# Kernel tuning notes

Hardware: AMD Instinct MI355X
Metric: run time of the kernel (lower is better)

The kernel has to match this reference:

```python
import jax, jax.numpy as jnp
import numpy as np

B, N, H, E, WF = 2048, 30, 256, 256, 32
TANH_C = 10.0  # tanh_exploration


def _mask_modify(m):
    # if a row is all True, un-mask the last column
    all_true = jnp.all(m, axis=1)
    return m.at[:, -1].set(m[:, -1] & ~all_true)


def _lstm_cell(x, h, c, W_ih, W_hh, b_ih, b_hh):
    gates = x @ W_ih.T + b_ih + h @ W_hh.T + b_hh
    i, f, g, o = jnp.split(gates, 4, axis=1)  # torch LSTMCell gate order
    c_new = jax.nn.sigmoid(f) * c + jax.nn.sigmoid(i) * jnp.tanh(g)
    h_new = jax.nn.sigmoid(o) * jnp.tanh(c_new)
    return h_new, c_new


def _attention(query, ref, Wq, bq, Wr, br, v, C=None):
    # query [B,H], ref [B,H,N] (context permuted)
    q = query @ Wq.T + bq                                        # [B,H]
    e = jnp.einsum('oh,bhn->bon', Wr, ref) + br[None, :, None]   # 1x1 conv
    u = jnp.einsum('h,bhn->bn', v, jnp.tanh(q[:, :, None] + e))  # [B,N]
    logits = C * jnp.tanh(u) if C is not None else u
    return e, logits


def setup_inputs() -> dict:
    key = jax.random.key(0)
    ks = jax.random.split(key, 24)
    s = 0.06  # ~1/sqrt(H) init scale
    n = lambda k, sh: jax.random.normal(k, sh, dtype=jnp.float32)
    return {
        'decoder_input': n(ks[0], (B, E)),
        'embedded_inputs': n(ks[1], (N, B, E)),
        'h0': n(ks[2], (B, H)),
        'c0': n(ks[3], (B, H)),
        'context': n(ks[4], (N, B, H)),
        'embed_cou': n(ks[5], (B, WF)),
        'D': jax.random.uniform(ks[6], (B, N, N), dtype=jnp.float32),
        'W_ih': n(ks[7], (4 * H, E)) * s,
        'W_hh': n(ks[8], (4 * H, H)) * s,
        'b_ih': n(ks[9], (4 * H,)) * s,
        'b_hh': n(ks[10], (4 * H,)) * s,
        'W_merge': n(ks[11], (H, H + WF)) * s,
        'b_merge': n(ks[12], (H,)) * s,
        'Wq_p': n(ks[13], (H, H)) * s,
        'bq_p': n(ks[14], (H,)) * s,
        'Wr_p': n(ks[15], (H, H)) * s,
        'br_p': n(ks[16], (H,)) * s,
        'v_p': n(ks[17], (H,)) * s,
        'Wq_g': n(ks[18], (H, H)) * s,
        'bq_g': n(ks[19], (H,)) * s,
        'Wr_g': n(ks[20], (H, H)) * s,
        'br_g': n(ks[21], (H,)) * s,
        'v_g': n(ks[22], (H,)) * s,
        'V_reach_mask_t': jnp.zeros((B, N), dtype=bool),
        'start_idx': jax.random.randint(ks[23], (B,), 0, N),
        'k_min_nodes': 3,
    }


def reference(decoder_input, embedded_inputs, h0, c0, context, embed_cou, D,
              W_ih, W_hh, b_ih, b_hh, W_merge, b_merge,
              Wq_p, bq_p, Wr_p, br_p, v_p,
              Wq_g, bq_g, Wr_g, br_g, v_g,
              V_reach_mask_t, start_idx, k_min_nodes):
    ref = jnp.transpose(context, (1, 2, 0))  # [B,H,N]
    arangeB = jnp.arange(B)
    arangeN = jnp.arange(N)

    def step(carry, _):
        h, c, mask, idxs, dec_in, knn_row = carry
        # --- update_knn_mask ('n-1'): builds the row used at the NEXT step ---
        Eb = D[arangeB, idxs]                                  # [B,N]
        weighted = Eb * (~mask).astype(Eb.dtype)
        valid = jnp.sum(~mask, axis=1) > k_min_nodes
        far = jnp.argmax(weighted, axis=1)
        next_row = (arangeN[None, :] == far[:, None]) & valid[:, None]
        # --- recurrence: update_mask + check_mask ---
        lm = mask.at[arangeB, idxs].set(True)
        lm = _mask_modify(_mask_modify(lm))
        full_mask = lm | knn_row
        # LSTM step + worker-feature merge
        hy, cy = _lstm_cell(dec_in, h, c, W_ih, W_hh, b_ih, b_hh)
        g_l = jnp.concatenate([hy, embed_cou], axis=1) @ W_merge.T + b_merge
        # one glimpse (n_glimpses=1)
        e_g, lg = _attention(g_l, ref, Wq_g, bq_g, Wr_g, br_g, v_g)
        lg = jnp.where(full_mask, -jnp.inf, lg)
        g_l = jnp.einsum('bhn,bn->bh', e_g, jax.nn.softmax(lg, axis=1))
        # pointer (use_tanh with C)
        _, lp = _attention(g_l, ref, Wq_p, bq_p, Wr_p, br_p, v_p, C=TANH_C)
        lp = jnp.where(full_mask, -jnp.inf, lp)
        log_p = jax.nn.log_softmax(lp, axis=1)
        new_idxs = jnp.argmax(log_p, axis=1)  # greedy decode
        new_dec = embedded_inputs[new_idxs, arangeB]  # [B,E]
        return (hy, cy, lm, new_idxs, new_dec, next_row), (log_p, new_idxs)

    init = (h0, c0, V_reach_mask_t, start_idx, decoder_input,
            jnp.zeros_like(V_reach_mask_t))
    (_, _, mask, _, _, _), (logps, sels) = jax.lax.scan(step, init, None, length=N)
    return jnp.swapaxes(logps, 0, 1), jnp.swapaxes(sels, 0, 1), mask
```

## Files before the change

### kernel.cpp

```cpp
#include <hip/hip_runtime.h>
#include <hip/hip_bf16.h>
#include <math.h>

#define B 2048
#define NN 30
#define H 256
#define EDIM 256
#define G4 1024

typedef __attribute__((ext_vector_type(8))) short short8;
typedef __attribute__((ext_vector_type(4))) float f32x4;

__device__ __forceinline__ float fsig(float x) {
    return __fdividef(1.f, 1.f + __expf(-x));
}
__device__ __forceinline__ float ftanh(float x) {
    return 1.f - __fdividef(2.f, __expf(2.f * x) + 1.f);
}

__device__ __forceinline__ void split3(float a, unsigned short& h,
                                       unsigned short& m_, unsigned short& l_)
{
    unsigned ab = __float_as_uint(a);
    h = (unsigned short)(ab >> 16);
    float r1 = a - __uint_as_float(ab & 0xffff0000u);
    unsigned rb = __float_as_uint(r1);
    m_ = (unsigned short)(rb >> 16);
    float r2 = r1 - __uint_as_float(rb & 0xffff0000u);
    l_ = (unsigned short)(__float_as_uint(r2) >> 16);
}

__global__ __launch_bounds__(256)
void gemm_big(const float* __restrict__ A,
              const float* __restrict__ W0, const float* __restrict__ W1,
              const float* __restrict__ W2,
              const float* __restrict__ b0, const float* __restrict__ b1,
              const float* __restrict__ b2,
              float* __restrict__ C0, float* __restrict__ C1,
              float* __restrict__ C2)
{
    __shared__ __align__(16) unsigned short Ah[128][40];
    __shared__ __align__(16) unsigned short Am[128][40];
    __shared__ __align__(16) unsigned short Al[128][40];
    __shared__ __align__(16) unsigned short Bh[128][40];
    __shared__ __align__(16) unsigned short Bm[128][40];
    __shared__ __align__(16) unsigned short Bl[128][40];

    int tid = threadIdx.x;
    int w = tid >> 6, l = tid & 63;

    int lin = blockIdx.y * 6 + blockIdx.x;
    int v = (lin & 7) * 360 + (lin >> 3);
    int m0 = (v / 6) << 7;
    int nblk = v % 6;
    int part = nblk >> 1;
    int nin = (nblk & 1) << 7;
    const float* W    = part == 0 ? W0 : part == 1 ? W1 : W2;
    const float* bias = part == 0 ? b0 : part == 1 ? b1 : b2;
    float* C          = part == 0 ? C0 : part == 1 ? C1 : C2;

    int srow = tid >> 1;
    int skb  = (tid & 1) << 4;
    const float* arow = A + (long)(m0 + srow) * 256 + skb;
    const float* wrow = W + (long)(nin + srow) * 256 + skb;

    int fr = l & 15;
    int fk = (l >> 4) << 3;

    f32x4 acc[2][8];
    #pragma unroll
    for (int i = 0; i < 2; ++i)
        #pragma unroll
        for (int j = 0; j < 8; ++j)
            acc[i][j] = (f32x4){0.f, 0.f, 0.f, 0.f};

    for (int kt = 0; kt < 8; ++kt) {
        int k0 = kt << 5;
        float4 a4[4], w4[4];
        #pragma unroll
        for (int i = 0; i < 4; ++i) {
            a4[i] = *(const float4*)(arow + k0 + (i << 2));
            w4[i] = *(const float4*)(wrow + k0 + (i << 2));
        }
        __syncthreads();
        #pragma unroll
        for (int i = 0; i < 4; ++i) {
            float va[4] = {a4[i].x, a4[i].y, a4[i].z, a4[i].w};
            float vw[4] = {w4[i].x, w4[i].y, w4[i].z, w4[i].w};
            #pragma unroll
            for (int j = 0; j < 4; ++j) {
                int c = skb + (i << 2) + j;
                split3(va[j], Ah[srow][c], Am[srow][c], Al[srow][c]);
                split3(vw[j], Bh[srow][c], Bm[srow][c], Bl[srow][c]);
            }
        }
        __syncthreads();

        short8 aH[2], aM[2], aL[2];
        #pragma unroll
        for (int ms = 0; ms < 2; ++ms) {
            int r = (w << 5) + (ms << 4) + fr;
            aH[ms] = *(const short8*)&Ah[r][fk];
            aM[ms] = *(const short8*)&Am[r][fk];
            aL[ms] = *(const short8*)&Al[r][fk];
        }
        #pragma unroll
        for (int ng = 0; ng < 2; ++ng) {
            short8 bH[4], bM[4], bL[4];
            #pragma unroll
            for (int j = 0; j < 4; ++j) {
                int r = (((ng << 2) + j) << 4) + fr;
                bH[j] = *(const short8*)&Bh[r][fk];
                bM[j] = *(const short8*)&Bm[r][fk];
                bL[j] = *(const short8*)&Bl[r][fk];
            }
            #pragma unroll
            for (int ms = 0; ms < 2; ++ms)
                #pragma unroll
                for (int j = 0; j < 4; ++j)
                    acc[ms][(ng << 2) + j] = __builtin_amdgcn_mfma_f32_16x16x32_bf16(
                        aH[ms], bH[j], acc[ms][(ng << 2) + j], 0, 0, 0);
            #pragma unroll
            for (int ms = 0; ms < 2; ++ms)
                #pragma unroll
                for (int j = 0; j < 4; ++j)
                    acc[ms][(ng << 2) + j] = __builtin_amdgcn_mfma_f32_16x16x32_bf16(
                        aH[ms], bM[j], acc[ms][(ng << 2) + j], 0, 0, 0);
            #pragma unroll
            for (int ms = 0; ms < 2; ++ms)
                #pragma unroll
                for (int j = 0; j < 4; ++j)
                    acc[ms][(ng << 2) + j] = __builtin_amdgcn_mfma_f32_16x16x32_bf16(
                        aM[ms], bH[j], acc[ms][(ng << 2) + j], 0, 0, 0);
            #pragma unroll
            for (int ms = 0; ms < 2; ++ms)
                #pragma unroll
                for (int j = 0; j < 4; ++j)
                    acc[ms][(ng << 2) + j] = __builtin_amdgcn_mfma_f32_16x16x32_bf16(
                        aH[ms], bL[j], acc[ms][(ng << 2) + j], 0, 0, 0);
            #pragma unroll
            for (int ms = 0; ms < 2; ++ms)
                #pragma unroll
                for (int j = 0; j < 4; ++j)
                    acc[ms][(ng << 2) + j] = __builtin_amdgcn_mfma_f32_16x16x32_bf16(
                        aM[ms], bM[j], acc[ms][(ng << 2) + j], 0, 0, 0);
            #pragma unroll
            for (int ms = 0; ms < 2; ++ms)
                #pragma unroll
                for (int j = 0; j < 4; ++j)
                    acc[ms][(ng << 2) + j] = __builtin_amdgcn_mfma_f32_16x16x32_bf16(
                        aL[ms], bH[j], acc[ms][(ng << 2) + j], 0, 0, 0);
        }
    }

    #pragma unroll
    for (int ms = 0; ms < 2; ++ms) {
        #pragma unroll
        for (int ns = 0; ns < 8; ++ns) {
            float bv = bias[nin + (ns << 4) + fr];
            #pragma unroll
            for (int r = 0; r < 4; ++r) {
                int m = m0 + (w << 5) + (ms << 4) + ((l >> 4) << 2) + r;
                C[(long)m * 256 + nin + (ns << 4) + fr] = acc[ms][ns][r] + bv;
            }
        }
    }
}

__global__ __launch_bounds__(256)
void gates_mfma(const unsigned short* __restrict__ dhi, const unsigned short* __restrict__ dlo,
                const unsigned short* __restrict__ hhi, const unsigned short* __restrict__ hlo,
                const unsigned short* __restrict__ Whi, const unsigned short* __restrict__ Wlo,
                const float* __restrict__ bsum, const float* __restrict__ cin,
                float* __restrict__ hout, float* __restrict__ cout,
                unsigned short* __restrict__ hohi, unsigned short* __restrict__ holo)
{
    __shared__ __align__(16) unsigned short Ah[128][40];
    __shared__ __align__(16) unsigned short Al[128][40];
    __shared__ __align__(16) unsigned short Bh[64][40];
    __shared__ __align__(16) unsigned short Bl[64][40];

    int tid = threadIdx.x;
    int w = tid >> 6, l = tid & 63;
    int lin = blockIdx.x;
    int v = (lin & 7) * 32 + (lin >> 3);
    int m0 = (v >> 4) << 7;
    int u0 = (v & 15) << 4;

    int arow = tid >> 1;
    int akb  = (tid & 1) << 4;
    int brw  = tid >> 2;
    int bkb  = (tid & 3) << 3;
    int wrow = ((brw >> 4) << 8) + u0 + (brw & 15);
    const unsigned short* wph = Whi + (long)wrow * 512 + bkb;
    const unsigned short* wpl = Wlo + (long)wrow * 512 + bkb;

    int fk = (l >> 4) << 3;
    int fr = l & 15;

    f32x4 acc[2][4];
    #pragma unroll
    for (int i = 0; i < 2; ++i)
        #pragma unroll
        for (int j = 0; j < 4; ++j)
            acc[i][j] = (f32x4){0.f, 0.f, 0.f, 0.f};

    for (int kt = 0; kt < 16; ++kt) {
        int k0 = kt << 5;
        const unsigned short* sah; const unsigned short* sal; int kk;
        if (k0 < 256) { sah = dhi; sal = dlo; kk = k0; }
        else          { sah = hhi; sal = hlo; kk = k0 - 256; }
        long abase = (long)(m0 + arow) * 256 + kk + akb;
        short8 a0 = *(const short8*)&sah[abase];
        short8 a1 = *(const short8*)&sah[abase + 8];
        short8 a2 = *(const short8*)&sal[abase];
        short8 a3 = *(const short8*)&sal[abase + 8];
        short8 b0 = *(const short8*)&wph[k0];
        short8 b1 = *(const short8*)&wpl[k0];
        __syncthreads();
        *(short8*)&Ah[arow][akb]     = a0;
        *(short8*)&Ah[arow][akb + 8] = a1;
        *(short8*)&Al[arow][akb]     = a2;
        *(short8*)&Al[arow][akb + 8] = a3;
        *(short8*)&Bh[brw][bkb] = b0;
        *(short8*)&Bl[brw][bkb] = b1;
        __syncthreads();

        short8 aH[2], aL[2], bH[4], bL[4];
        #pragma unroll
        for (int ms = 0; ms < 2; ++ms) {
            int r = (w << 5) + (ms << 4) + fr;
            aH[ms] = *(const short8*)&Ah[r][fk];
            aL[ms] = *(const short8*)&Al[r][fk];
        }
        #pragma unroll
        for (int s = 0; s < 4; ++s) {
            int r = (s << 4) + fr;
            bH[s] = *(const short8*)&Bh[r][fk];
            bL[s] = *(const short8*)&Bl[r][fk];
        }
        #pragma unroll
        for (int ms = 0; ms < 2; ++ms)
            #pragma unroll
            for (int s = 0; s < 4; ++s)
                acc[ms][s] = __builtin_amdgcn_mfma_f32_16x16x32_bf16(aH[ms], bH[s], acc[ms][s], 0, 0, 0);
        #pragma unroll
        for (int ms = 0; ms < 2; ++ms)
            #pragma unroll
            for (int s = 0; s < 4; ++s)
                acc[ms][s] = __builtin_amdgcn_mfma_f32_16x16x32_bf16(aH[ms], bL[s], acc[ms][s], 0, 0, 0);
        #pragma unroll
        for (int ms = 0; ms < 2; ++ms)
            #pragma unroll
            for (int s = 0; s < 4; ++s)
                acc[ms][s] = __builtin_amdgcn_mfma_f32_16x16x32_bf16(aL[ms], bH[s], acc[ms][s], 0, 0, 0);
    }

    int u = u0 + fr;
    float bI = bsum[u], bF = bsum[256 + u], bG = bsum[512 + u], bO = bsum[768 + u];
    #pragma unroll
    for (int ms = 0; ms < 2; ++ms) {
        #pragma unroll
        for (int r = 0; r < 4; ++r) {
            int m = m0 + (w << 5) + (ms << 4) + ((l >> 4) << 2) + r;
            float gi = acc[ms][0][r] + bI;
            float gf = acc[ms][1][r] + bF;
            float gg = acc[ms][2][r] + bG;
            float go = acc[ms][3][r] + bO;
            float cv = cin[(long)m * H + u];
            float cn = fsig(gf) * cv + fsig(gi) * ftanh(gg);
            float hn = fsig(go) * ftanh(cn);
            cout[(long)m * H + u] = cn;
            hout[(long)m * H + u] = hn;
            unsigned hb = __float_as_uint(hn);
            hohi[(long)m * H + u] = (unsigned short)(hb >> 16);
            float lo = hn - __uint_as_float(hb & 0xffff0000u);
            holo[(long)m * H + u] = (unsigned short)(__float_as_uint(lo) >> 16);
        }
    }
}

__global__ __launch_bounds__(256)
void gemm_qg(const float* __restrict__ A, const float* __restrict__ W,
             const float* __restrict__ addend, float* __restrict__ C)
{
    __shared__ __align__(16) float As[2][16][36];
    __shared__ __align__(16) float Ws[2][16][68];
    int tid = threadIdx.x;
    int tx = tid & 15, ty = tid >> 4;

    int lin = blockIdx.y * 4 + blockIdx.x;
    int v = (lin & 7) * 32 + (lin >> 3);
    int m0 = (v >> 2) << 5;
    int n0 = (v & 3) << 6;

    int lrA = tid >> 3, lkA = (tid & 7) << 1;
    int lrW = tid >> 2, lkW = (tid & 3) << 2;
    const float* arow = A + (long)(m0 + lrA) * 256;
    const float* wrow = W + (long)(n0 + lrW) * 256;

    float2 av = *(const float2*)(arow + lkA);
    float4 wv = *(const float4*)(wrow + lkW);
    As[0][lkA + 0][lrA] = av.x; As[0][lkA + 1][lrA] = av.y;
    Ws[0][lkW + 0][lrW] = wv.x; Ws[0][lkW + 1][lrW] = wv.y;
    Ws[0][lkW + 2][lrW] = wv.z; Ws[0][lkW + 3][lrW] = wv.w;
    __syncthreads();

    float acc[2][4] = {};
    int p = 0;
    for (int k0 = 0; k0 < 256; k0 += 16) {
        float2 nav; float4 nwv;
        bool more = (k0 + 16) < 256;
        if (more) {
            nav = *(const float2*)(arow + k0 + 16 + lkA);
            nwv = *(const float4*)(wrow + k0 + 16 + lkW);
        }
        #pragma unroll
        for (int k = 0; k < 16; ++k) {
            float2 a2 = *(const float2*)&As[p][k][ty << 1];
            float4 b4 = *(const float4*)&Ws[p][k][tx << 2];
            acc[0][0] = fmaf(a2.x, b4.x, acc[0][0]);
            acc[0][1] = fmaf(a2.x, b4.y, acc[0][1]);
            acc[0][2] = fmaf(a2.x, b4.z, acc[0][2]);
            acc[0][3] = fmaf(a2.x, b4.w, acc[0][3]);
            acc[1][0] = fmaf(a2.y, b4.x, acc[1][0]);
            acc[1][1] = fmaf(a2.y, b4.y, acc[1][1]);
            acc[1][2] = fmaf(a2.y, b4.z, acc[1][2]);
            acc[1][3] = fmaf(a2.y, b4.w, acc[1][3]);
        }
        if (more) {
            int q = p ^ 1;
            As[q][lkA + 0][lrA] = nav.x; As[q][lkA + 1][lrA] = nav.y;
            Ws[q][lkW + 0][lrW] = nwv.x; Ws[q][lkW + 1][lrW] = nwv.y;
            Ws[q][lkW + 2][lrW] = nwv.z; Ws[q][lkW + 3][lrW] = nwv.w;
        }
        __syncthreads();
        p ^= 1;
    }

    #pragma unroll
    for (int i = 0; i < 2; ++i) {
        int m = m0 + (ty << 1) + i;
        const float* ad = &addend[(long)m * 256 + n0 + (tx << 2)];
        float4 adv = *(const float4*)ad;
        float4 o = make_float4(acc[i][0] + adv.x, acc[i][1] + adv.y,
                               acc[i][2] + adv.z, acc[i][3] + adv.w);
        *(float4*)&C[(long)m * 256 + n0 + (tx << 2)] = o;
    }
}

__global__ void init_state(const unsigned char* __restrict__ vr, const int* __restrict__ start,
                           unsigned char* __restrict__ mask, unsigned char* __restrict__ knn,
                           int* __restrict__ idxs)
{
    int t = blockIdx.x * 256 + threadIdx.x;
    if (t < B * NN) { mask[t] = vr[t] ? 1 : 0; knn[t] = 0; }
    if (t < B) idxs[t] = start[t];
}

__global__ void prep_wsplit(const float* __restrict__ Wih, const float* __restrict__ Whh,
                            const float* __restrict__ bih, const float* __restrict__ bhh,
                            unsigned short* __restrict__ Whi, unsigned short* __restrict__ Wlo,
                            float* __restrict__ bsum)
{
    int n = blockIdx.x, k = threadIdx.x;
    float a = Wih[(long)n * H + k];
    unsigned ab = __float_as_uint(a);
    Whi[(long)n * 512 + k] = (unsigned short)(ab >> 16);
    float alo = a - __uint_as_float(ab & 0xffff0000u);
    Wlo[(long)n * 512 + k] = (unsigned short)(__float_as_uint(alo) >> 16);
    float b = Whh[(long)n * H + k];
    unsigned bb = __float_as_uint(b);
    Whi[(long)n * 512 + 256 + k] = (unsigned short)(bb >> 16);
    float blo = b - __uint_as_float(bb & 0xffff0000u);
    Wlo[(long)n * 512 + 256 + k] = (unsigned short)(__float_as_uint(blo) >> 16);
    if (k == 0) bsum[n] = bih[n] + bhh[n];
}

__global__ void conv_pair(const float* __restrict__ x,
                          unsigned short* __restrict__ xhi, unsigned short* __restrict__ xlo)
{
    int t = blockIdx.x * 256 + threadIdx.x;
    float a = x[t];
    unsigned ab = __float_as_uint(a);
    xhi[t] = (unsigned short)(ab >> 16);
    float lo = a - __uint_as_float(ab & 0xffff0000u);
    xlo[t] = (unsigned short)(__float_as_uint(lo) >> 16);
}

__global__ void prep_compose1(const float* __restrict__ Wqg, const float* __restrict__ Wm,
                              float* __restrict__ W1c)
{
    int h = blockIdx.x, k = threadIdx.x;
    float a = 0.f;
    for (int j = 0; j < H; ++j) a = fmaf(Wqg[(long)h * H + j], Wm[(long)j * 288 + k], a);
    W1c[(long)h * H + k] = a;
}

__global__ void prep_compose2(const float* __restrict__ Wqg, const float* __restrict__ Wm,
                              const float* __restrict__ bm, const float* __restrict__ bqg,
                              float* __restrict__ W2c, float* __restrict__ bc)
{
    int h = blockIdx.x, w = threadIdx.x;
    if (w < 32) {
        float a = 0.f;
        for (int j = 0; j < H; ++j) a = fmaf(Wqg[(long)h * H + j], Wm[(long)j * 288 + 256 + w], a);
        W2c[h * 32 + w] = a;
    } else if (w == 32) {
        float a = 0.f;
        for (int j = 0; j < H; ++j) a = fmaf(Wqg[(long)h * H + j], bm[j], a);
        bc[h] = a + bqg[h];
    }
}

__global__ __launch_bounds__(256)
void prep_qc(const float* __restrict__ cou, const float* __restrict__ W2c,
             const float* __restrict__ bc, float* __restrict__ qc)
{
    __shared__ float sWT[32 * 256];
    __shared__ float sb[256];
    int b = blockIdx.x, h = threadIdx.x;
    for (int i = h; i < 32 * 256; i += 256) {
        int hh = i >> 5, ww = i & 31;
        sWT[ww * 256 + hh] = W2c[i];
    }
    sb[h] = bc[h];
    __syncthreads();
    const float* cr = cou + (long)b * 32;
    float a = sb[h];
    for (int w = 0; w < 32; ++w) a = fmaf(cr[w], sWT[w * 256 + h], a);
    qc[(long)b * H + h] = a;
}

__global__ void prep_composeF(const float* __restrict__ Wqp, const float* __restrict__ Wrg,
                              const float* __restrict__ brg, float* __restrict__ WFc,
                              float* __restrict__ bFc)
{
    int f = blockIdx.x, k = threadIdx.x;
    float a = 0.f;
    for (int j = 0; j < H; ++j) a = fmaf(Wqp[(long)f * H + j], Wrg[(long)j * H + k], a);
    WFc[(long)f * H + k] = a;
    if (k == 0) {
        float s = 0.f;
        for (int j = 0; j < H; ++j) s = fmaf(Wqp[(long)f * H + j], brg[j], s);
        bFc[f] = s;
    }
}

__global__ __launch_bounds__(512)
void mega_attn2(const float* __restrict__ eg, const float* __restrict__ ep,
                const float* __restrict__ F, const float* __restrict__ qg,
                const float* __restrict__ vg, const float* __restrict__ vp,
                const float* __restrict__ bqp,
                const float* __restrict__ D, const int* __restrict__ kminp,
                unsigned char* __restrict__ mask, unsigned char* __restrict__ knn,
                const float* __restrict__ emb,
                float* __restrict__ out, int step,
                int* __restrict__ idxs,
                unsigned short* __restrict__ dechi, unsigned short* __restrict__ declo)
{
    int b = blockIdx.x, tid = threadIdx.x;
    int wv = tid >> 6, lane = tid & 63;
    __shared__ float sU[32], sP[32];
    __shared__ float sQp[H];
    __shared__ float sPar[2][H];
    __shared__ unsigned char sFull[32];
    __shared__ int sSel;

    float4 q4  = ((const float4*)(qg + (long)b * H))[lane];
    float4 vg4 = ((const float4*)vg)[lane];
    float4 vp4 = ((const float4*)vp)[lane];

    if (tid < 64) {
        bool in = lane < NN;
        int idx = idxs[b];
        int kmin = *kminp;
        unsigned char m = in ? mask[b * NN + lane] : (unsigned char)1;
        float dv = in ? D[((long)b * NN + idx) * NN + lane] : 0.f;
        unsigned long long unm = __ballot(in && !m);
        int cnt = __popcll(unm);
        bool valid = cnt > kmin;
        float bw = (in && !m) ? dv : (in ? 0.f : -1.f);
        int bi = in ? lane : 1000;
        #pragma unroll
        for (int off = 32; off; off >>= 1) {
            float ow = __shfl_down(bw, off, 64);
            int oi = __shfl_down(bi, off, 64);
            if (ow > bw || (ow == bw && oi < bi)) { bw = ow; bi = oi; }
        }
        int far = __shfl(bi, 0, 64);
        unsigned char mnew = (in && lane == idx) ? 1 : m;
        #pragma unroll
        for (int rep = 0; rep < 2; ++rep) {
            bool allm = (__ballot(in && !mnew) == 0ull);
            if (allm && lane == NN - 1) mnew = 0;
        }
        unsigned char kn = in ? knn[b * NN + lane] : 0;
        if (in) {
            sFull[lane] = (mnew | kn) ? 1 : 0;
            mask[b * NN + lane] = mnew;
            knn[b * NN + lane] = (lane == far && valid) ? 1 : 0;
        }
    }
    __syncthreads();

    for (int n = wv; n < NN; n += 8) {
        if (sFull[n]) continue;
        float4 e4 = ((const float4*)(eg + ((long)n * B + b) * H))[lane];
        float s = vg4.x * ftanh(q4.x + e4.x);
        s = fmaf(vg4.y, ftanh(q4.y + e4.y), s);
        s = fmaf(vg4.z, ftanh(q4.z + e4.z), s);
        s = fmaf(vg4.w, ftanh(q4.w + e4.w), s);
        #pragma unroll
        for (int off = 32; off; off >>= 1) s += __shfl_down(s, off, 64);
        if (lane == 0) sU[n] = s;
    }
    __syncthreads();

    if (tid < 64) {
        bool in = tid < NN;
        bool f = in ? (sFull[tid] != 0) : true;
        float u = (in && !f) ? sU[tid] : -INFINITY;
        float mx = u;
        #pragma unroll
        for (int off = 32; off; off >>= 1) mx = fmaxf(mx, __shfl_down(mx, off, 64));
        mx = __shfl(mx, 0, 64);
        float p = (in && !f) ? __expf(u - mx) : 0.f;
        float sum = p;
        #pragma unroll
        for (int off = 32; off; off >>= 1) sum += __shfl_down(sum, off, 64);
        sum = __shfl(sum, 0, 64);
        if (in) sP[tid] = p / sum;
    }
    __syncthreads();

    {
        int half = tid >> 8, hh = tid & 255;
        float a = 0.f;
        #pragma unroll
        for (int n = 0; n < 15; ++n) {
            int nn = half * 15 + n;
            float pn = sP[nn];
            if (pn != 0.f)
                a = fmaf(pn, F[((long)nn * B + b) * H + hh], a);
        }
        sPar[half][hh] = a;
    }
    __syncthreads();
    if (tid < 256) sQp[tid] = bqp[tid] + sPar[0][tid] + sPar[1][tid];
    __syncthreads();

    float4 qp4 = ((const float4*)sQp)[lane];
    for (int n = wv; n < NN; n += 8) {
        if (sFull[n]) continue;
        float4 e4 = ((const float4*)(ep + ((long)n * B + b) * H))[lane];
        float s = vp4.x * ftanh(qp4.x + e4.x);
        s = fmaf(vp4.y, ftanh(qp4.y + e4.y), s);
        s = fmaf(vp4.z, ftanh(qp4.z + e4.z), s);
        s = fmaf(vp4.w, ftanh(qp4.w + e4.w), s);
        #pragma unroll
        for (int off = 32; off; off >>= 1) s += __shfl_down(s, off, 64);
        if (lane == 0) sU[n] = 10.f * ftanh(s);
    }
    __syncthreads();

    if (tid < 64) {
        bool in = tid < NN;
        bool f = in ? (sFull[tid] != 0) : true;
        float l = (in && !f) ? sU[tid] : -INFINITY;
        float mx = l; int bi = in ? tid : 1000;
        #pragma unroll
        for (int off = 32; off; off >>= 1) {
            float om = __shfl_down(mx, off, 64);
            int oi = __shfl_down(bi, off, 64);
            if (om > mx || (om == mx && oi < bi)) { mx = om; bi = oi; }
        }
        mx = __shfl(mx, 0, 64);
        bi = __shfl(bi, 0, 64);
        float pe = (in && !f) ? __expf(l - mx) : 0.f;
        float sum = pe;
        #pragma unroll
        for (int off = 32; off; off >>= 1) sum += __shfl_down(sum, off, 64);
        sum = __shfl(sum, 0, 64);
        float lse = mx + __logf(sum);
        if (tid == 0) {
            idxs[b] = bi;
            out[(long)B * NN * NN + (long)b * NN + step] = (float)bi;
            sSel = bi;
        }
        if (in)
            out[(long)b * NN * NN + (long)step * NN + tid] =
                f ? -1e30f : (l - lse);
    }
    __syncthreads();

    if (tid < 256) {
        int sel = sSel;
        float d = emb[((long)sel * B + b) * EDIM + tid];
        unsigned db = __float_as_uint(d);
        dechi[(long)b * H + tid] = (unsigned short)(db >> 16);
        float lo = d - __uint_as_float(db & 0xffff0000u);
        declo[(long)b * H + tid] = (unsigned short)(__float_as_uint(lo) >> 16);
    }
}

__global__ void mask_out(const unsigned char* __restrict__ mask, float* __restrict__ out)
{
    int t = blockIdx.x * 256 + threadIdx.x;
    if (t < B * NN)
        out[(long)B * NN * NN + (long)B * NN + t] = mask[t] ? 1.f : 0.f;
}

extern "C" void kernel_launch(void* const* d_in, const int* in_sizes, int n_in,
                              void* d_out, int out_size, void* d_ws, size_t ws_size,
                              hipStream_t stream)
{
    const float* decoder_input = (const float*)d_in[0];
    const float* embedded     = (const float*)d_in[1];
    const float* h0           = (const float*)d_in[2];
    const float* c0           = (const float*)d_in[3];
    const float* context      = (const float*)d_in[4];
    const float* embed_cou    = (const float*)d_in[5];
    const float* D            = (const float*)d_in[6];
    const float* W_ih         = (const float*)d_in[7];
    const float* W_hh         = (const float*)d_in[8];
    const float* b_ih         = (const float*)d_in[9];
    const float* b_hh         = (const float*)d_in[10];
    const float* W_merge      = (const float*)d_in[11];
    const float* b_merge      = (const float*)d_in[12];
    const float* Wq_p         = (const float*)d_in[13];
    const float* bq_p         = (const float*)d_in[14];
    const float* Wr_p         = (const float*)d_in[15];
    const float* br_p         = (const float*)d_in[16];
    const float* v_p          = (const float*)d_in[17];
    const float* Wq_g         = (const float*)d_in[18];
    const float* bq_g         = (const float*)d_in[19];
    const float* Wr_g         = (const float*)d_in[20];
    const float* br_g         = (const float*)d_in[21];
    const float* v_g          = (const float*)d_in[22];
    const unsigned char* vreach = (const unsigned char*)d_in[23];
    const int* start_idx      = (const int*)d_in[24];
    const int* kminp          = (const int*)d_in[25];

    float* ws = (float*)d_ws;
    size_t o = 0;
    float* eg     = ws + o; o += (size_t)B * NN * H;
    float* ep     = ws + o; o += (size_t)B * NN * H;
    float* Fbuf   = ws + o; o += (size_t)B * NN * H;
    float* hb0    = ws + o; o += (size_t)B * H;
    float* hb1    = ws + o; o += (size_t)B * H;
    float* cb0    = ws + o; o += (size_t)B * H;
    float* cb1    = ws + o; o += (size_t)B * H;
    float* qbuf   = ws + o; o += (size_t)B * H;
    float* qc     = ws + o; o += (size_t)B * H;
    float* W1c    = ws + o; o += (size_t)H * H;
    float* W2c    = ws + o; o += (size_t)H * 32;
    float* bc     = ws + o; o += (size_t)H;
    float* WFc    = ws + o; o += (size_t)H * H;
    float* bFc    = ws + o; o += (size_t)H;
    float* bsum   = ws + o; o += (size_t)G4;
    unsigned short* Whi  = (unsigned short*)(ws + o); o += (size_t)G4 * 512 / 2;
    unsigned short* Wlo  = (unsigned short*)(ws + o); o += (size_t)G4 * 512 / 2;
    unsigned short* dechi = (unsigned short*)(ws + o); o += (size_t)B * H / 2;
    unsigned short* declo = (unsigned short*)(ws + o); o += (size_t)B * H / 2;
    unsigned short* hAhi = (unsigned short*)(ws + o); o += (size_t)B * H / 2;
    unsigned short* hAlo = (unsigned short*)(ws + o); o += (size_t)B * H / 2;
    unsigned short* hBhi = (unsigned short*)(ws + o); o += (size_t)B * H / 2;
    unsigned short* hBlo = (unsigned short*)(ws + o); o += (size_t)B * H / 2;
    unsigned char* maskb = (unsigned char*)(ws + o);
    unsigned char* knnb  = maskb + (size_t)B * NN;
    int* idxs = (int*)(knnb + (size_t)B * NN + 64);

    float* out = (float*)d_out;

    init_state<<<dim3((B * NN + 255) / 256), dim3(256), 0, stream>>>(
        vreach, start_idx, maskb, knnb, idxs);

    prep_wsplit<<<dim3(G4), dim3(256), 0, stream>>>(W_ih, W_hh, b_ih, b_hh,
                                                    Whi, Wlo, bsum);
    conv_pair<<<dim3(B * H / 256), dim3(256), 0, stream>>>(decoder_input, dechi, declo);
    conv_pair<<<dim3(B * H / 256), dim3(256), 0, stream>>>(h0, hAhi, hAlo);
    prep_compose1<<<dim3(H), dim3(256), 0, stream>>>(Wq_g, W_merge, W1c);
    prep_compose2<<<dim3(H), dim3(64), 0, stream>>>(Wq_g, W_merge, b_merge, bq_g,
                                                    W2c, bc);
    prep_qc<<<dim3(B), dim3(256), 0, stream>>>(embed_cou, W2c, bc, qc);
    prep_composeF<<<dim3(H), dim3(256), 0, stream>>>(Wq_p, Wr_g, br_g, WFc, bFc);

    gemm_big<<<dim3(6, (B * NN) / 128), dim3(256), 0, stream>>>(
        context, Wr_g, Wr_p, WFc, br_g, br_p, bFc, eg, ep, Fbuf);

    const float* cin = c0;
    unsigned short* hInHi = hAhi; unsigned short* hInLo = hAlo;
    unsigned short* hOutHi = hBhi; unsigned short* hOutLo = hBlo;

    for (int step = 0; step < NN; ++step) {
        int p = step & 1;
        float* hout = p ? hb1 : hb0;
        float* cout = p ? cb1 : cb0;

        gates_mfma<<<dim3(256), dim3(256), 0, stream>>>(
            dechi, declo, hInHi, hInLo, Whi, Wlo, bsum, cin,
            hout, cout, hOutHi, hOutLo);

        gemm_qg<<<dim3(4, B / 32), dim3(256), 0, stream>>>(
            hout, W1c, qc, qbuf);

        mega_attn2<<<dim3(B), dim3(512), 0, stream>>>(
            eg, ep, Fbuf, qbuf, v_g, v_p, bq_p, D, kminp,
            maskb, knnb, embedded, out, step, idxs, dechi, declo);

        cin = cout;
        unsigned short* th = hInHi; hInHi = hOutHi; hOutHi = th;
        unsigned short* tl = hInLo; hInLo = hOutLo; hOutLo = tl;
    }

    mask_out<<<dim3((B * NN + 255) / 256), dim3(256), 0, stream>>>(maskb, out);
}
```

Before: 2.383 ms.

## Fuse glimpse query GEMM into attention kernel, batch four rows per block

Removes the per-step gemm_qg launch. The hy@W1c product is now computed inside the attention kernel from a transposed composed weight, with each 512-thread block serving four batch rows (two waves per row) instead of one. Separately, the three projection weights for the big context GEMM are pre-split once into bf16 hi/mid/lo arrays, so the GEMM no longer re-splits them for every tile. This saves a launch and a qbuf round trip per step and reduces GEMM split work. In exchange, each attention block now reads the full 256x256 W1cT from global memory, which adds per-block weight traffic.

```diff
diff --git a/kernel.cpp b/kernel.cpp
--- a/kernel.cpp
+++ b/kernel.cpp
@@ -32,8 +32,8 @@
 
 __global__ __launch_bounds__(256)
 void gemm_big(const float* __restrict__ A,
-              const float* __restrict__ W0, const float* __restrict__ W1,
-              const float* __restrict__ W2,
+              const unsigned short* __restrict__ Wh, const unsigned short* __restrict__ Wm,
+              const unsigned short* __restrict__ Wl,
               const float* __restrict__ b0, const float* __restrict__ b1,
               const float* __restrict__ b2,
               float* __restrict__ C0, float* __restrict__ C1,
@@ -55,14 +55,16 @@
     int nblk = v % 6;
     int part = nblk >> 1;
     int nin = (nblk & 1) << 7;
-    const float* W    = part == 0 ? W0 : part == 1 ? W1 : W2;
     const float* bias = part == 0 ? b0 : part == 1 ? b1 : b2;
     float* C          = part == 0 ? C0 : part == 1 ? C1 : C2;
+    long woff = (long)part * 65536;
 
     int srow = tid >> 1;
     int skb  = (tid & 1) << 4;
     const float* arow = A + (long)(m0 + srow) * 256 + skb;
-    const float* wrow = W + (long)(nin + srow) * 256 + skb;
+    const unsigned short* wph = Wh + woff + (long)(nin + srow) * 256 + skb;
+    const unsigned short* wpm = Wm + woff + (long)(nin + srow) * 256 + skb;
+    const unsigned short* wpl = Wl + woff + (long)(nin + srow) * 256 + skb;
 
     int fr = l & 15;
     int fk = (l >> 4) << 3;
@@ -76,24 +78,32 @@
 
     for (int kt = 0; kt < 8; ++kt) {
         int k0 = kt << 5;
-        float4 a4[4], w4[4];
-        #pragma unroll
-        for (int i = 0; i < 4; ++i) {
+        float4 a4[4];
+        #pragma unroll
+        for (int i = 0; i < 4; ++i)
             a4[i] = *(const float4*)(arow + k0 + (i << 2));
-            w4[i] = *(const float4*)(wrow + k0 + (i << 2));
-        }
+        short8 wh0 = *(const short8*)(wph + k0);
+        short8 wh1 = *(const short8*)(wph + k0 + 8);
+        short8 wm0 = *(const short8*)(wpm + k0);
+        short8 wm1 = *(const short8*)(wpm + k0 + 8);
+        short8 wl0 = *(const short8*)(wpl + k0);
+        short8 wl1 = *(const short8*)(wpl + k0 + 8);
         __syncthreads();
         #pragma unroll
         for (int i = 0; i < 4; ++i) {
             float va[4] = {a4[i].x, a4[i].y, a4[i].z, a4[i].w};
-            float vw[4] = {w4[i].x, w4[i].y, w4[i].z, w4[i].w};
             #pragma unroll
             for (int j = 0; j < 4; ++j) {
                 int c = skb + (i << 2) + j;
                 split3(va[j], Ah[srow][c], Am[srow][c], Al[srow][c]);
-                split3(vw[j], Bh[srow][c], Bm[srow][c], Bl[srow][c]);
             }
         }
+        *(short8*)&Bh[srow][skb]     = wh0;
+        *(short8*)&Bh[srow][skb + 8] = wh1;
+        *(short8*)&Bm[srow][skb]     = wm0;
+        *(short8*)&Bm[srow][skb + 8] = wm1;
+        *(short8*)&Bl[srow][skb]     = wl0;
+        *(short8*)&Bl[srow][skb + 8] = wl1;
         __syncthreads();
 
         short8 aH[2], aM[2], aL[2];
@@ -280,75 +290,6 @@
     }
 }
 
-__global__ __launch_bounds__(256)
-void gemm_qg(const float* __restrict__ A, const float* __restrict__ W,
-             const float* __restrict__ addend, float* __restrict__ C)
-{
-    __shared__ __align__(16) float As[2][16][36];
-    __shared__ __align__(16) float Ws[2][16][68];
-    int tid = threadIdx.x;
-    int tx = tid & 15, ty = tid >> 4;
-
-    int lin = blockIdx.y * 4 + blockIdx.x;
-    int v = (lin & 7) * 32 + (lin >> 3);
-    int m0 = (v >> 2) << 5;
-    int n0 = (v & 3) << 6;
-
-    int lrA = tid >> 3, lkA = (tid & 7) << 1;
-    int lrW = tid >> 2, lkW = (tid & 3) << 2;
-    const float* arow = A + (long)(m0 + lrA) * 256;
-    const float* wrow = W + (long)(n0 + lrW) * 256;
-
-    float2 av = *(const float2*)(arow + lkA);
-    float4 wv = *(const float4*)(wrow + lkW);
-    As[0][lkA + 0][lrA] = av.x; As[0][lkA + 1][lrA] = av.y;
-    Ws[0][lkW + 0][lrW] = wv.x; Ws[0][lkW + 1][lrW] = wv.y;
-    Ws[0][lkW + 2][lrW] = wv.z; Ws[0][lkW + 3][lrW] = wv.w;
-    __syncthreads();
-
-    float acc[2][4] = {};
-    int p = 0;
-    for (int k0 = 0; k0 < 256; k0 += 16) {
-        float2 nav; float4 nwv;
-        bool more = (k0 + 16) < 256;
-        if (more) {
-            nav = *(const float2*)(arow + k0 + 16 + lkA);
-            nwv = *(const float4*)(wrow + k0 + 16 + lkW);
-        }
-        #pragma unroll
-        for (int k = 0; k < 16; ++k) {
-            float2 a2 = *(const float2*)&As[p][k][ty << 1];
-            float4 b4 = *(const float4*)&Ws[p][k][tx << 2];
-            acc[0][0] = fmaf(a2.x, b4.x, acc[0][0]);
-            acc[0][1] = fmaf(a2.x, b4.y, acc[0][1]);
-            acc[0][2] = fmaf(a2.x, b4.z, acc[0][2]);
-            acc[0][3] = fmaf(a2.x, b4.w, acc[0][3]);
-            acc[1][0] = fmaf(a2.y, b4.x, acc[1][0]);
-            acc[1][1] = fmaf(a2.y, b4.y, acc[1][1]);
-            acc[1][2] = fmaf(a2.y, b4.z, acc[1][2]);
-            acc[1][3] = fmaf(a2.y, b4.w, acc[1][3]);
-        }
-        if (more) {
-            int q = p ^ 1;
-            As[q][lkA + 0][lrA] = nav.x; As[q][lkA + 1][lrA] = nav.y;
-            Ws[q][lkW + 0][lrW] = nwv.x; Ws[q][lkW + 1][lrW] = nwv.y;
-            Ws[q][lkW + 2][lrW] = nwv.z; Ws[q][lkW + 3][lrW] = nwv.w;
-        }
-        __syncthreads();
-        p ^= 1;
-    }
-
-    #pragma unroll
-    for (int i = 0; i < 2; ++i) {
-        int m = m0 + (ty << 1) + i;
-        const float* ad = &addend[(long)m * 256 + n0 + (tx << 2)];
-        float4 adv = *(const float4*)ad;
-        float4 o = make_float4(acc[i][0] + adv.x, acc[i][1] + adv.y,
-                               acc[i][2] + adv.z, acc[i][3] + adv.w);
-        *(float4*)&C[(long)m * 256 + n0 + (tx << 2)] = o;
-    }
-}
-
 __global__ void init_state(const unsigned char* __restrict__ vr, const int* __restrict__ start,
                            unsigned char* __restrict__ mask, unsigned char* __restrict__ knn,
                            int* __restrict__ idxs)
@@ -377,6 +318,19 @@
     if (k == 0) bsum[n] = bih[n] + bhh[n];
 }
 
+__global__ void prep_splitW(const float* __restrict__ W0, const float* __restrict__ W1,
+                            const float* __restrict__ W2,
+                            unsigned short* __restrict__ Wh, unsigned short* __restrict__ Wm,
+                            unsigned short* __restrict__ Wl)
+{
+    int id = blockIdx.x;
+    int p = id >> 8, r = id & 255, k = threadIdx.x;
+    const float* W = p == 0 ? W0 : p == 1 ? W1 : W2;
+    float a = W[(long)r * 256 + k];
+    long o = (long)p * 65536 + (long)r * 256 + k;
+    split3(a, Wh[o], Wm[o], Wl[o]);
+}
+
 __global__ void conv_pair(const float* __restrict__ x,
                           unsigned short* __restrict__ xhi, unsigned short* __restrict__ xlo)
 {
@@ -389,12 +343,12 @@
 }
 
 __global__ void prep_compose1(const float* __restrict__ Wqg, const float* __restrict__ Wm,
-                              float* __restrict__ W1c)
+                              float* __restrict__ W1cT)
 {
     int h = blockIdx.x, k = threadIdx.x;
     float a = 0.f;
     for (int j = 0; j < H; ++j) a = fmaf(Wqg[(long)h * H + j], Wm[(long)j * 288 + k], a);
-    W1c[(long)h * H + k] = a;
+    W1cT[(long)k * H + h] = a;
 }
 
 __global__ void prep_compose2(const float* __restrict__ Wqg, const float* __restrict__ Wm,
@@ -448,30 +402,56 @@
 }
 
 __global__ __launch_bounds__(512)
-void mega_attn2(const float* __restrict__ eg, const float* __restrict__ ep,
-                const float* __restrict__ F, const float* __restrict__ qg,
-                const float* __restrict__ vg, const float* __restrict__ vp,
-                const float* __restrict__ bqp,
-                const float* __restrict__ D, const int* __restrict__ kminp,
-                unsigned char* __restrict__ mask, unsigned char* __restrict__ knn,
-                const float* __restrict__ emb,
-                float* __restrict__ out, int step,
-                int* __restrict__ idxs,
-                unsigned short* __restrict__ dechi, unsigned short* __restrict__ declo)
-{
-    int b = blockIdx.x, tid = threadIdx.x;
+void mega8(const float* __restrict__ eg, const float* __restrict__ ep,
+           const float* __restrict__ F, const float* __restrict__ hout,
+           const float* __restrict__ qc, const float* __restrict__ W1cT,
+           const float* __restrict__ vg, const float* __restrict__ vp,
+           const float* __restrict__ bqp,
+           const float* __restrict__ D, const int* __restrict__ kminp,
+           unsigned char* __restrict__ mask, unsigned char* __restrict__ knn,
+           const float* __restrict__ emb,
+           float* __restrict__ out, int step,
+           int* __restrict__ idxs,
+           unsigned short* __restrict__ dechi, unsigned short* __restrict__ declo)
+{
+    __shared__ float sHy[4][256];
+    __shared__ float sQg[4][256];
+    __shared__ float sU[4][32];
+    __shared__ unsigned char sFull[4][32];
+
+    int tid = threadIdx.x;
     int wv = tid >> 6, lane = tid & 63;
-    __shared__ float sU[32], sP[32];
-    __shared__ float sQp[H];
-    __shared__ float sPar[2][H];
-    __shared__ unsigned char sFull[32];
-    __shared__ int sSel;
-
-    float4 q4  = ((const float4*)(qg + (long)b * H))[lane];
-    float4 vg4 = ((const float4*)vg)[lane];
-    float4 vp4 = ((const float4*)vp)[lane];
-
-    if (tid < 64) {
+    int pi = wv >> 1, sub = wv & 1;
+    int blk = blockIdx.x;
+    int vB = (blk & 7) * 64 + (blk >> 3);
+    int b0 = vB << 2;
+    int b = b0 + pi;
+
+    #pragma unroll
+    for (int i = 0; i < 2; ++i) {
+        int idx2 = tid + (i << 9);
+        int bl = idx2 >> 8, hh = idx2 & 255;
+        sHy[bl][hh] = hout[(long)(b0 + bl) * H + hh];
+    }
+    __syncthreads();
+
+    {
+        int hh = tid & 255, g = tid >> 8;
+        float a0 = 0.f, a1 = 0.f;
+        const float* wp = W1cT + hh;
+        const float* h0p = sHy[(g << 1)];
+        const float* h1p = sHy[(g << 1) + 1];
+        #pragma unroll 4
+        for (int k = 0; k < 256; ++k) {
+            float wval = wp[(long)k * H];
+            a0 = fmaf(h0p[k], wval, a0);
+            a1 = fmaf(h1p[k], wval, a1);
+        }
+        sQg[(g << 1)][hh]     = qc[(long)(b0 + (g << 1)) * H + hh] + a0;
+        sQg[(g << 1) + 1][hh] = qc[(long)(b0 + (g << 1) + 1) * H + hh] + a1;
+    }
+
+    if (sub == 0) {
         bool in = lane < NN;
         int idx = idxs[b];
         int kmin = *kminp;
@@ -497,62 +477,70 @@
         }
         unsigned char kn = in ? knn[b * NN + lane] : 0;
         if (in) {
-            sFull[lane] = (mnew | kn) ? 1 : 0;
+            sFull[pi][lane] = (mnew | kn) ? 1 : 0;
             mask[b * NN + lane] = mnew;
             knn[b * NN + lane] = (lane == far && valid) ? 1 : 0;
         }
     }
     __syncthreads();
 
-    for (int n = wv; n < NN; n += 8) {
-        if (sFull[n]) continue;
-        float4 e4 = ((const float4*)(eg + ((long)n * B + b) * H))[lane];
-        float s = vg4.x * ftanh(q4.x + e4.x);
-        s = fmaf(vg4.y, ftanh(q4.y + e4.y), s);
-        s = fmaf(vg4.z, ftanh(q4.z + e4.z), s);
-        s = fmaf(vg4.w, ftanh(q4.w + e4.w), s);
-        #pragma unroll
-        for (int off = 32; off; off >>= 1) s += __shfl_down(s, off, 64);
-        if (lane == 0) sU[n] = s;
+    float4 vg4 = ((const float4*)vg)[lane];
+    float4 vp4 = ((const float4*)vp)[lane];
+
+    {
+        float4 q4 = ((const float4*)&sQg[pi][0])[lane];
+        for (int n = sub; n < NN; n += 2) {
+            if (sFull[pi][n]) continue;
+            float4 e4 = ((const float4*)(eg + ((long)n * B + b) * H))[lane];
+            float s = vg4.x * ftanh(q4.x + e4.x);
+            s = fmaf(vg4.y, ftanh(q4.y + e4.y), s);
+            s = fmaf(vg4.z, ftanh(q4.z + e4.z), s);
+            s = fmaf(vg4.w, ftanh(q4.w + e4.w), s);
+            #pragma unroll
+            for (int off = 32; off; off >>= 1) s += __shfl_down(s, off, 64);
+            if (lane == 0) sU[pi][n] = s;
+        }
     }
     __syncthreads();
 
-    if (tid < 64) {
-        bool in = tid < NN;
-        bool f = in ? (sFull[tid] != 0) : true;
-        float u = (in && !f) ? sU[tid] : -INFINITY;
+    float pr;
+    {
+        bool in = lane < NN;
+        bool fm = in ? (sFull[pi][lane] != 0) : true;
+        float u = (in && !fm) ? sU[pi][lane] : -INFINITY;
         float mx = u;
         #pragma unroll
         for (int off = 32; off; off >>= 1) mx = fmaxf(mx, __shfl_down(mx, off, 64));
         mx = __shfl(mx, 0, 64);
-        float p = (in && !f) ? __expf(u - mx) : 0.f;
+        float p = (in && !fm) ? __expf(u - mx) : 0.f;
         float sum = p;
         #pragma unroll
         for (int off = 32; off; off >>= 1) sum += __shfl_down(sum, off, 64);
         sum = __shfl(sum, 0, 64);
-        if (in) sP[tid] = p / sum;
+        pr = p / sum;
+    }
+
+    float4 qp4;
+    {
+        float4 qa = {0.f, 0.f, 0.f, 0.f};
+        #pragma unroll
+        for (int n = 0; n < NN; ++n) {
+            float pn = __shfl(pr, n, 64);
+            if (pn != 0.f) {
+                float4 F4 = ((const float4*)(F + ((long)n * B + b) * H))[lane];
+                qa.x = fmaf(pn, F4.x, qa.x);
+                qa.y = fmaf(pn, F4.y, qa.y);
+                qa.z = fmaf(pn, F4.z, qa.z);
+                qa.w = fmaf(pn, F4.w, qa.w);
+            }
+        }
+        float4 bq4 = ((const float4*)bqp)[lane];
+        qp4 = make_float4(bq4.x + qa.x, bq4.y + qa.y, bq4.z + qa.z, bq4.w + qa.w);
     }
     __syncthreads();
 
-    {
-        int half = tid >> 8, hh = tid & 255;
-        float a = 0.f;
-        #pragma unroll
-        for (int n = 0; n < 15; ++n) {
-            int nn = half * 15 + n;
-            float pn = sP[nn];
-            if (pn != 0.f)
-                a = fmaf(pn, F[((long)nn * B + b) * H + hh], a);
-        }
-        sPar[half][hh] = a;
-    }
-    __syncthreads();
-    if (tid < 256) sQp[tid] = bqp[tid] + sPar[0][tid] + sPar[1][tid];
-    __syncthreads();
-
-    float4 qp4 = ((const float4*)sQp)[lane];
-    for (int n = wv; n < NN; n += 8) {
-        if (sFull[n]) continue;
+    for (int n = sub; n < NN; n += 2) {
+        if (sFull[pi][n]) continue;
         float4 e4 = ((const float4*)(ep + ((long)n * B + b) * H))[lane];
         float s = vp4.x * ftanh(qp4.x + e4.x);
         s = fmaf(vp4.y, ftanh(qp4.y + e4.y), s);
@@ -560,15 +548,15 @@
         s = fmaf(vp4.w, ftanh(qp4.w + e4.w), s);
         #pragma unroll
         for (int off = 32; off; off >>= 1) s += __shfl_down(s, off, 64);
-        if (lane == 0) sU[n] = 10.f * ftanh(s);
+        if (lane == 0) sU[pi][n] = 10.f * ftanh(s);
     }
     __syncthreads();
 
-    if (tid < 64) {
-        bool in = tid < NN;
-        bool f = in ? (sFull[tid] != 0) : true;
-        float l = (in && !f) ? sU[tid] : -INFINITY;
-        float mx = l; int bi = in ? tid : 1000;
+    {
+        bool in = lane < NN;
+        bool fm = in ? (sFull[pi][lane] != 0) : true;
+        float lg = (in && !fm) ? sU[pi][lane] : -INFINITY;
+        float mx = lg; int bi = in ? lane : 1000;
         #pragma unroll
         for (int off = 32; off; off >>= 1) {
             float om = __shfl_down(mx, off, 64);
@@ -577,30 +565,32 @@
         }
         mx = __shfl(mx, 0, 64);
         bi = __shfl(bi, 0, 64);
-        float pe = (in && !f) ? __expf(l - mx) : 0.f;
+        float pe = (in && !fm) ? __expf(lg - mx) : 0.f;
         float sum = pe;
         #pragma unroll
         for (int off = 32; off; off >>= 1) sum += __shfl_down(sum, off, 64);
         sum = __shfl(sum, 0, 64);
         float lse = mx + __logf(sum);
-        if (tid == 0) {
-            idxs[b] = bi;
-            out[(long)B * NN * NN + (long)b * NN + step] = (float)bi;
-            sSel = bi;
-        }
-        if (in)
-            out[(long)b * NN * NN + (long)step * NN + tid] =
-                f ? -1e30f : (l - lse);
-    }
-    __syncthreads();
-
-    if (tid < 256) {
-        int sel = sSel;
-        float d = emb[((long)sel * B + b) * EDIM + tid];
-        unsigned db = __float_as_uint(d);
-        dechi[(long)b * H + tid] = (unsigned short)(db >> 16);
-        float lo = d - __uint_as_float(db & 0xffff0000u);
-        declo[(long)b * H + tid] = (unsigned short)(__float_as_uint(lo) >> 16);
+        if (sub == 0) {
+            if (lane == 0) {
+                idxs[b] = bi;
+                out[(long)B * NN * NN + (long)b * NN + step] = (float)bi;
+            }
+            if (in)
+                out[(long)b * NN * NN + (long)step * NN + lane] =
+                    fm ? -1e30f : (lg - lse);
+        }
+        int sel = bi;
+        int hbase = lane + (sub ? 128 : 0);
+        #pragma unroll
+        for (int j = 0; j < 2; ++j) {
+            int hh = hbase + (j << 6);
+            float d = emb[((long)sel * B + b) * EDIM + hh];
+            unsigned db = __float_as_uint(d);
+            dechi[(long)b * H + hh] = (unsigned short)(db >> 16);
+            float lo = d - __uint_as_float(db & 0xffff0000u);
+            declo[(long)b * H + hh] = (unsigned short)(__float_as_uint(lo) >> 16);
+        }
     }
 }
 
@@ -651,9 +641,8 @@
     float* hb1    = ws + o; o += (size_t)B * H;
     float* cb0    = ws + o; o += (size_t)B * H;
     float* cb1    = ws + o; o += (size_t)B * H;
-    float* qbuf   = ws + o; o += (size_t)B * H;
     float* qc     = ws + o; o += (size_t)B * H;
-    float* W1c    = ws + o; o += (size_t)H * H;
+    float* W1cT   = ws + o; o += (size_t)H * H;
     float* W2c    = ws + o; o += (size_t)H * 32;
     float* bc     = ws + o; o += (size_t)H;
     float* WFc    = ws + o; o += (size_t)H * H;
@@ -661,6 +650,9 @@
     float* bsum   = ws + o; o += (size_t)G4;
     unsigned short* Whi  = (unsigned short*)(ws + o); o += (size_t)G4 * 512 / 2;
     unsigned short* Wlo  = (unsigned short*)(ws + o); o += (size_t)G4 * 512 / 2;
+    unsigned short* Wsh  = (unsigned short*)(ws + o); o += (size_t)3 * 65536 / 2;
+    unsigned short* Wsm  = (unsigned short*)(ws + o); o += (size_t)3 * 65536 / 2;
+    unsigned short* Wsl  = (unsigned short*)(ws + o); o += (size_t)3 * 65536 / 2;
     unsigned short* dechi = (unsigned short*)(ws + o); o += (size_t)B * H / 2;
     unsigned short* declo = (unsigned short*)(ws + o); o += (size_t)B * H / 2;
     unsigned short* hAhi = (unsigned short*)(ws + o); o += (size_t)B * H / 2;
@@ -680,14 +672,16 @@
                                                     Whi, Wlo, bsum);
     conv_pair<<<dim3(B * H / 256), dim3(256), 0, stream>>>(decoder_input, dechi, declo);
     conv_pair<<<dim3(B * H / 256), dim3(256), 0, stream>>>(h0, hAhi, hAlo);
-    prep_compose1<<<dim3(H), dim3(256), 0, stream>>>(Wq_g, W_merge, W1c);
+    prep_compose1<<<dim3(H), dim3(256), 0, stream>>>(Wq_g, W_merge, W1cT);
     prep_compose2<<<dim3(H), dim3(64), 0, stream>>>(Wq_g, W_merge, b_merge, bq_g,
                                                     W2c, bc);
     prep_qc<<<dim3(B), dim3(256), 0, stream>>>(embed_cou, W2c, bc, qc);
     prep_composeF<<<dim3(H), dim3(256), 0, stream>>>(Wq_p, Wr_g, br_g, WFc, bFc);
+    prep_splitW<<<dim3(3 * 256), dim3(256), 0, stream>>>(Wr_g, Wr_p, WFc,
+                                                         Wsh, Wsm, Wsl);
 
     gemm_big<<<dim3(6, (B * NN) / 128), dim3(256), 0, stream>>>(
-        context, Wr_g, Wr_p, WFc, br_g, br_p, bFc, eg, ep, Fbuf);
+        context, Wsh, Wsm, Wsl, br_g, br_p, bFc, eg, ep, Fbuf);
 
     const float* cin = c0;
     unsigned short* hInHi = hAhi; unsigned short* hInLo = hAlo;
@@ -702,11 +696,8 @@
             dechi, declo, hInHi, hInLo, Whi, Wlo, bsum, cin,
             hout, cout, hOutHi, hOutLo);
 
-        gemm_qg<<<dim3(4, B / 32), dim3(256), 0, stream>>>(
-            hout, W1c, qc, qbuf);
-
-        mega_attn2<<<dim3(B), dim3(512), 0, stream>>>(
-            eg, ep, Fbuf, qbuf, v_g, v_p, bq_p, D, kminp,
+        mega8<<<dim3(B / 4), dim3(512), 0, stream>>>(
+            eg, ep, Fbuf, hout, qc, W1cT, v_g, v_p, bq_p, D, kminp,
             maskb, knnb, embedded, out, step, idxs, dechi, declo);
 
         cin = cout;
```

Result: faster. 2.233 ms (-6.3%).
